# Optimization experiments

Measured on AMD Instinct MI355X. Metric: run time of the kernel, lower is better.

The kernel has to match this reference:

```python
import jax, jax.numpy as jnp
import numpy as np

MIN_NORM = 1e-15
PROJ_EPS = 4e-3  # hgcn PoincareBall eps for float32
C = 1.0          # curvature (constant across both layers)


def _norm(x):
    return jnp.clip(jnp.linalg.norm(x, axis=-1, keepdims=True), MIN_NORM)


def _artanh(x):
    return jnp.arctanh(jnp.clip(x, -1.0 + 1e-7, 1.0 - 1e-7))


def proj(x, c):
    # clip points inside the Poincare ball of curvature c
    n = _norm(x)
    maxnorm = (1.0 - PROJ_EPS) / jnp.sqrt(c)
    return jnp.where(n > maxnorm, x / n * maxnorm, x)


def expmap0(u, c):
    sc = jnp.sqrt(c)
    n = _norm(u)
    return jnp.tanh(sc * n) * u / (sc * n)


def logmap0(p, c):
    sc = jnp.sqrt(c)
    n = _norm(p)
    return _artanh(sc * n) * p / (sc * n)


def mobius_add(x, y, c):
    x2 = jnp.sum(x * x, -1, keepdims=True)
    y2 = jnp.sum(y * y, -1, keepdims=True)
    xy = jnp.sum(x * y, -1, keepdims=True)
    num = (1.0 + 2.0 * c * xy + c * y2) * x + (1.0 - c * x2) * y
    den = 1.0 + 2.0 * c * xy + (c ** 2) * x2 * y2
    return num / jnp.clip(den, MIN_NORM)


def mobius_matvec(W, x, c):
    sc = jnp.sqrt(c)
    xn = _norm(x)
    mx = x @ W.T
    mxn = _norm(mx)
    res = jnp.tanh(mxn / xn * _artanh(sc * xn)) * mx / (mxn * sc)
    zero = jnp.all(mx == 0, axis=-1, keepdims=True)
    return jnp.where(zero, jnp.zeros((), x.dtype), res)


def hgc_layer(x, W, b, src, dst, ew, c_in, c_out, N):
    # HypLinear: mobius matvec + hyperbolic bias
    h = proj(mobius_matvec(W, x, c_in), c_in)
    hyp_b = proj(expmap0(b[None, :], c_in), c_in)  # proj_tan0 is identity
    h = proj(mobius_add(h, hyp_b, c_in), c_in)
    # HypAgg: tangent-space sparse aggregation
    xt = logmap0(h, c_in)                               # [N, d]
    msg = ew[:, None] * xt[src]                          # [E, d] gather
    agg = jax.ops.segment_sum(msg, dst, num_segments=N)  # spmm(adj, xt)
    h = proj(expmap0(agg, c_in), c_in)
    # HypAct: relu in tangent space, remap with c_out
    xt = jax.nn.relu(logmap0(h, c_in))
    return proj(expmap0(xt, c_out), c_out)


def setup_inputs() -> dict:
    key = jax.random.key(0)
    ks = jax.random.split(key, 8)
    N, F, H, D, E = 100000, 128, 128, 128, 1600000
    s = 1.0 / np.sqrt(F)
    x = jax.random.normal(ks[0], (N, F), jnp.float32) * 0.1
    W1 = jax.random.normal(ks[1], (H, F), jnp.float32) * s
    b1 = jax.random.normal(ks[2], (H,), jnp.float32) * 0.01
    W2 = jax.random.normal(ks[3], (D, H), jnp.float32) * s
    b2 = jax.random.normal(ks[4], (D,), jnp.float32) * 0.01
    edge_weight = jax.random.uniform(ks[5], (E,), jnp.float32) * (1.0 / 16.0)
    src = jax.random.randint(ks[6], (E,), 0, N)
    dst = jax.random.randint(ks[7], (E,), 0, N)
    return {"x": x, "W1": W1, "b1": b1, "W2": W2, "b2": b2,
            "edge_weight": edge_weight, "src": src, "dst": dst}


def reference(x, W1, b1, W2, b2, edge_weight, src, dst):
    N = x.shape[0]
    # HGCN.encode: map Euclidean features onto the manifold
    xh = proj(expmap0(x, C), C)  # proj_tan0 is identity for PoincareBall
    h = hgc_layer(xh, W1, b1, src, dst, edge_weight, C, C, N)
    h = hgc_layer(h, W2, b2, src, dst, edge_weight, C, C, N)
    return h
```

## Files before the change

kernel.cpp:

```cpp
#include <hip/hip_runtime.h>
#include <hip/hip_bf16.h>

#define MINN 1e-15f
#define MAXN (1.0f - 4e-3f)
#define ATMAX 3.1063031f

#define NBH 9
#define BNODES 512
#define BCAP 10240
#define BWIN (BCAP + 4 * BNODES)
#define PBE 8192

typedef short short8 __attribute__((ext_vector_type(8)));
typedef float f32x4 __attribute__((ext_vector_type(4)));

__device__ __forceinline__ float wsum(float v) {
    v += __shfl_xor(v, 32, 64);
    v += __shfl_xor(v, 16, 64);
    v += __shfl_xor(v, 8, 64);
    v += __shfl_xor(v, 4, 64);
    v += __shfl_xor(v, 2, 64);
    v += __shfl_xor(v, 1, 64);
    return v;
}

__device__ __forceinline__ void splitf(float f, short& hi, short& lo) {
    unsigned u = __float_as_uint(f);
    hi = (short)(u >> 16);
    float r = f - __uint_as_float(u & 0xffff0000u);
    lo = (short)(__float_as_uint(r) >> 16);
}

__device__ __forceinline__ unsigned packsplit_hi(short ha, short hb) {
    return (unsigned)(unsigned short)ha | ((unsigned)(unsigned short)hb << 16);
}

__device__ __forceinline__ unsigned pack_bf16(float a, float b) {
    unsigned ua = __float_as_uint(a);
    unsigned ub = __float_as_uint(b);
    ua = (ua + 0x7fffu + ((ua >> 16) & 1u)) >> 16;
    ub = (ub + 0x7fffu + ((ub >> 16) & 1u)) & 0xffff0000u;
    return ua | ub;
}

__device__ __forceinline__ float tanh_fast(float x) {
    float e = __expf(2.f * x);
    return (e - 1.f) * __builtin_amdgcn_rcpf(e + 1.f);
}
__device__ __forceinline__ float atanh_fast(float x) {
    return 0.5f * __logf((1.f + x) * __builtin_amdgcn_rcpf(1.f - x));
}

__global__ __launch_bounds__(256) void k_bucket(const int* __restrict__ src, const int* __restrict__ dst,
                                                const float* __restrict__ ew, int* __restrict__ gcur,
                                                int2* __restrict__ staging, int E, int NBUCK) {
    __shared__ int hist[512];
    const int tid = threadIdx.x;
    const int e0 = blockIdx.x * PBE;
    for (int i = tid; i < 512; i += 256) hist[i] = 0;
    __syncthreads();
    #pragma unroll 4
    for (int j = 0; j < PBE / 256; j++) {
        int e = e0 + j * 256 + tid;
        if (e < E) atomicAdd(&hist[dst[e] >> NBH], 1);
    }
    __syncthreads();
    for (int b = tid; b < NBUCK; b += 256) {
        int c = hist[b];
        hist[b] = c ? atomicAdd(&gcur[b], c) : 0;
    }
    __syncthreads();
    #pragma unroll 4
    for (int j = 0; j < PBE / 256; j++) {
        int e = e0 + j * 256 + tid;
        if (e < E) {
            int d = dst[e];
            int bkt = d >> NBH;
            int pos = atomicAdd(&hist[bkt], 1);
            if (pos < BCAP)
                staging[(size_t)bkt * BCAP + pos] =
                    make_int2((src[e] & 0x1FFFF) | ((d & (BNODES - 1)) << 17), __float_as_int(ew[e]));
        }
    }
}

__global__ __launch_bounds__(256) void k_cbuild(const int* __restrict__ gcur, const int2* __restrict__ staging,
                                                int2* __restrict__ csr, int2* __restrict__ rp2, int N) {
    __shared__ int cnt[BNODES];
    __shared__ int base[BNODES];
    __shared__ int sbuf[256];
    const int tid = threadIdx.x;
    const int b = blockIdx.x;
    const int bcnt = min(gcur[b], BCAP);
    const int wbase = b * BWIN;
    const int2* st = staging + (size_t)b * BCAP;

    for (int i = tid; i < BNODES; i += 256) cnt[i] = 0;
    __syncthreads();
    for (int i = tid; i < bcnt; i += 256) {
        int nl = (st[i].x >> 17) & (BNODES - 1);
        atomicAdd(&cnt[nl], 1);
    }
    __syncthreads();
    int p0 = (cnt[2 * tid] + 3) & ~3;
    int p1 = (cnt[2 * tid + 1] + 3) & ~3;
    int s = p0 + p1;
    sbuf[tid] = s;
    __syncthreads();
    for (int off = 1; off < 256; off <<= 1) {
        int add = (tid >= off) ? sbuf[tid - off] : 0;
        __syncthreads();
        sbuf[tid] += add;
        __syncthreads();
    }
    int excl = sbuf[tid] - s;
    base[2 * tid] = excl;
    base[2 * tid + 1] = excl + p0;
    __syncthreads();
    for (int i = tid; i < BNODES; i += 256) {
        int node = b * BNODES + i;
        int c = cnt[i];
        int pd = (c + 3) & ~3;
        int gb = wbase + base[i];
        if (node < N) rp2[node] = make_int2(gb, pd);
        for (int k = c; k < pd; k++) csr[gb + k] = make_int2(0, 0);
    }
    __syncthreads();
    for (int i = tid; i < BNODES; i += 256) cnt[i] = wbase + base[i];
    __syncthreads();
    for (int i = tid; i < bcnt; i += 256) {
        int2 p = st[i];
        int nl = (p.x >> 17) & (BNODES - 1);
        int pos = atomicAdd(&cnt[nl], 1);
        csr[pos] = make_int2(p.x & 0x1FFFF, p.y);
    }
}

__global__ __launch_bounds__(256) void k_wprep(const float* __restrict__ W1, const float* __restrict__ W2,
                                               unsigned* __restrict__ WH1, unsigned* __restrict__ WL1,
                                               unsigned* __restrict__ WH2, unsigned* __restrict__ WL2) {
    int i = (blockIdx.x & 31) * 256 + threadIdx.x;
    const float* W = (blockIdx.x < 32) ? W1 : W2;
    unsigned* WH = (blockIdx.x < 32) ? WH1 : WH2;
    unsigned* WL = (blockIdx.x < 32) ? WL1 : WL2;
    float a = W[2 * i], b = W[2 * i + 1];
    short ha, la, hb, lb;
    splitf(a, ha, la); splitf(b, hb, lb);
    WH[i] = packsplit_hi(ha, hb);
    WL[i] = packsplit_hi(la, lb);
}

__global__ __launch_bounds__(64) void k_bias(const float* __restrict__ B1, const float* __restrict__ B2,
                                             float2* __restrict__ HB) {
    const int lane = threadIdx.x;
    const float* B = (blockIdx.x == 0) ? B1 : B2;
    float2 bb = *(const float2*)(B + 2 * lane);
    float nb2 = wsum(bb.x * bb.x + bb.y * bb.y);
    float nb = fmaxf(sqrtf(nb2), MINN);
    float tbc = fminf(tanh_fast(nb), MAXN);
    float fb = tbc / nb;
    HB[blockIdx.x * 65 + lane] = make_float2(fb * bb.x, fb * bb.y);
    if (lane == 0) HB[blockIdx.x * 65 + 64] = make_float2(tbc * tbc, 0.f);
}

template <int ENCODE>
__global__ __launch_bounds__(256) void k_linear(
    const float* __restrict__ X,
    const unsigned* __restrict__ XH, const unsigned* __restrict__ XL,
    const unsigned* __restrict__ WH, const unsigned* __restrict__ WL,
    const float2* __restrict__ HB, const float2* __restrict__ NRM,
    unsigned* __restrict__ OUT, int N)
{
    __shared__ float mxs[4][16][132];
    __shared__ float xn2s[4][16];

    const int lane = threadIdx.x & 63;
    const int wid = threadIdx.x >> 6;
    const int lr = lane & 15;
    const int lg = lane >> 4;
    const int tbase = blockIdx.x * 4;

    short8 Bh[2][4], Bl[2][4];
    #pragma unroll
    for (int ct = 0; ct < 2; ct++) {
        const int nrow = wid * 32 + ct * 16 + lr;
        #pragma unroll
        for (int kt = 0; kt < 4; kt++) {
            Bh[ct][kt] = *(const short8*)(WH + nrow * 64 + kt * 16 + lg * 4);
            Bl[ct][kt] = *(const short8*)(WL + nrow * 64 + kt * 16 + lg * 4);
        }
    }
    float2 hb = HB[lane];
    float y2 = HB[64].x;

    #pragma unroll
    for (int t = 0; t < 4; t++) {
        const int row0 = (tbase + t) << 4;
        if (row0 >= N) break;
        const int arow = min(row0 + lr, N - 1);

        short8 Ah[4], Al[4];
        if (ENCODE) {
            float xn2 = 0.f;
            const float* xr = X + (size_t)arow * 128 + lg * 8;
            #pragma unroll
            for (int kt = 0; kt < 4; kt++) {
                float4 a0 = *(const float4*)(xr + kt * 32);
                float4 a1 = *(const float4*)(xr + kt * 32 + 4);
                float av[8] = {a0.x, a0.y, a0.z, a0.w, a1.x, a1.y, a1.z, a1.w};
                #pragma unroll
                for (int i = 0; i < 8; i++) {
                    xn2 = fmaf(av[i], av[i], xn2);
                    short h, l; splitf(av[i], h, l);
                    Ah[kt][i] = h; Al[kt][i] = l;
                }
            }
            xn2 += __shfl_xor(xn2, 16, 64);
            xn2 += __shfl_xor(xn2, 32, 64);
            if (wid == 0 && lane < 16) xn2s[t][lane] = xn2;
        } else {
            #pragma unroll
            for (int kt = 0; kt < 4; kt++) {
                Ah[kt] = *(const short8*)(XH + (size_t)arow * 64 + kt * 16 + lg * 4);
                Al[kt] = *(const short8*)(XL + (size_t)arow * 64 + kt * 16 + lg * 4);
            }
        }

        f32x4 acc0 = {0.f, 0.f, 0.f, 0.f}, acc1 = {0.f, 0.f, 0.f, 0.f};
        #pragma unroll
        for (int kt = 0; kt < 4; kt++) {
            acc0 = __builtin_amdgcn_mfma_f32_16x16x32_bf16(Ah[kt], Bh[0][kt], acc0, 0, 0, 0);
            acc1 = __builtin_amdgcn_mfma_f32_16x16x32_bf16(Ah[kt], Bh[1][kt], acc1, 0, 0, 0);
            acc0 = __builtin_amdgcn_mfma_f32_16x16x32_bf16(Al[kt], Bh[0][kt], acc0, 0, 0, 0);
            acc1 = __builtin_amdgcn_mfma_f32_16x16x32_bf16(Al[kt], Bh[1][kt], acc1, 0, 0, 0);
            acc0 = __builtin_amdgcn_mfma_f32_16x16x32_bf16(Ah[kt], Bl[0][kt], acc0, 0, 0, 0);
            acc1 = __builtin_amdgcn_mfma_f32_16x16x32_bf16(Ah[kt], Bl[1][kt], acc1, 0, 0, 0);
        }

        #pragma unroll
        for (int r = 0; r < 4; r++) {
            mxs[t][lg * 4 + r][wid * 32 + lr] = acc0[r];
            mxs[t][lg * 4 + r][wid * 32 + 16 + lr] = acc1[r];
        }
    }
    __syncthreads();

    float mn2[16], dmb[16];
    float2 mvv[16];
    #pragma unroll
    for (int t = 0; t < 4; t++) {
        #pragma unroll
        for (int r = 0; r < 4; r++) {
            const int q = t * 4 + r;
            mvv[q] = *(const float2*)&mxs[t][wid * 4 + r][2 * lane];
            mn2[q] = mvv[q].x * mvv[q].x + mvv[q].y * mvv[q].y;
            dmb[q] = mvv[q].x * hb.x + mvv[q].y * hb.y;
        }
    }
    #pragma unroll
    for (int s = 32; s; s >>= 1) {
        #pragma unroll
        for (int q = 0; q < 16; q++) {
            mn2[q] += __shfl_xor(mn2[q], s, 64);
            dmb[q] += __shfl_xor(dmb[q], s, 64);
        }
    }
    #pragma unroll
    for (int t = 0; t < 4; t++) {
        #pragma unroll
        for (int r = 0; r < 4; r++) {
            const int q = t * 4 + r;
            const int row = ((tbase + t) << 4) + wid * 4 + r;
            if (row < N) {
                float xn, axn;
                if (ENCODE) {
                    float n0 = fmaxf(sqrtf(xn2s[t][wid * 4 + r]), MINN);
                    xn = n0;
                    axn = fminf(n0, ATMAX);
                } else {
                    float2 nr = NRM[row];
                    xn = fmaxf(nr.x, MINN);
                    axn = nr.y;
                }
                float mxn = fmaxf(sqrtf(mn2[q]), MINN);
                float arg = (mxn / xn) * axn;
                float thc = fminf(tanh_fast(arg), MAXN);
                float f1 = thc / mxn;
                float x2 = thc * thc;
                float xy = f1 * dmb[q];
                float ca = 1.f + 2.f * xy + y2;
                float cb = 1.f - x2;
                float inv = 1.f / fmaxf(1.f + 2.f * xy + x2 * y2, MINN);
                float ng2 = inv * inv * (ca * ca * x2 + 2.f * ca * cb * xy + cb * cb * y2);
                float ng = fmaxf(sqrtf(ng2), MINN);
                float lf = atanh_fast(fminf(ng, MAXN)) / ng;
                float sle = lf * inv;
                float o0 = sle * (ca * f1 * mvv[q].x + cb * hb.x);
                float o1 = sle * (ca * f1 * mvv[q].y + cb * hb.y);
                OUT[(size_t)row * 64 + lane] = pack_bf16(o0, o1);
            }
        }
    }
}

__global__ __launch_bounds__(256) void k_aggact(const unsigned* __restrict__ XT, const int2* __restrict__ rp2,
                                                const int2* __restrict__ csr,
                                                float* __restrict__ OUTF,
                                                unsigned* __restrict__ OUTH, unsigned* __restrict__ OUTL,
                                                float2* __restrict__ NRM, int N, int last) {
    const int lane = threadIdx.x & 63;
    const int wid = threadIdx.x >> 6;
    int node = blockIdx.x * 4 + wid;
    if (node >= N) return;
    int2 rr = rp2[node];
    int b = __builtin_amdgcn_readfirstlane(rr.x);
    int cnt = __builtin_amdgcn_readfirstlane(rr.y);
    int e8 = b + (cnt & ~7);

    float ax[8], ay[8];
    #pragma unroll
    for (int j = 0; j < 8; j++) { ax[j] = 0.f; ay[j] = 0.f; }

    for (int i = b; i < e8; i += 8) {
        int2 c[8];
        #pragma unroll
        for (int j = 0; j < 8; j++) c[j] = csr[i + j];
        unsigned v[8];
        #pragma unroll
        for (int j = 0; j < 8; j++) v[j] = XT[(size_t)c[j].x * 64 + lane];
        #pragma unroll
        for (int j = 0; j < 8; j++) {
            float w = __int_as_float(c[j].y);
            ax[j] = fmaf(w, __uint_as_float(v[j] << 16), ax[j]);
            ay[j] = fmaf(w, __uint_as_float(v[j] & 0xffff0000u), ay[j]);
        }
    }
    if (cnt & 4) {
        int i = e8;
        int2 c[4];
        #pragma unroll
        for (int j = 0; j < 4; j++) c[j] = csr[i + j];
        unsigned v[4];
        #pragma unroll
        for (int j = 0; j < 4; j++) v[j] = XT[(size_t)c[j].x * 64 + lane];
        #pragma unroll
        for (int j = 0; j < 4; j++) {
            float w = __int_as_float(c[j].y);
            ax[j] = fmaf(w, __uint_as_float(v[j] << 16), ax[j]);
            ay[j] = fmaf(w, __uint_as_float(v[j] & 0xffff0000u), ay[j]);
        }
    }
    float a0 = ((ax[0] + ax[1]) + (ax[2] + ax[3])) + ((ax[4] + ax[5]) + (ax[6] + ax[7]));
    float a1 = ((ay[0] + ay[1]) + (ay[2] + ay[3])) + ((ay[4] + ay[5]) + (ay[6] + ay[7]));

    float r0 = fmaxf(a0, 0.f), r1 = fmaxf(a1, 0.f);
    float n2 = a0 * a0 + a1 * a1;
    float q2 = r0 * r0 + r1 * r1;
    #pragma unroll
    for (int s = 32; s; s >>= 1) {
        n2 += __shfl_xor(n2, s, 64);
        q2 += __shfl_xor(q2, s, 64);
    }
    float n = fmaxf(sqrtf(n2), MINN);
    float cp = fminf(n, ATMAX) / n;
    float nq = fmaxf(cp * sqrtf(q2), MINN);
    float tq = fminf(tanh_fast(nq), MAXN);
    float f2 = tq / nq;
    float sc = f2 * cp;
    float o0 = sc * r0, o1 = sc * r1;
    if (last) {
        *(float2*)(OUTF + (size_t)node * 128 + 2 * lane) = make_float2(o0, o1);
    } else {
        short h0, l0, h1, l1;
        splitf(o0, h0, l0); splitf(o1, h1, l1);
        OUTH[(size_t)node * 64 + lane] = packsplit_hi(h0, h1);
        OUTL[(size_t)node * 64 + lane] = packsplit_hi(l0, l1);
        if (lane == 0) NRM[node] = make_float2(tq, fminf(nq, ATMAX));
    }
}

extern "C" void kernel_launch(void* const* d_in, const int* in_sizes, int n_in,
                              void* d_out, int out_size, void* d_ws, size_t ws_size,
                              hipStream_t stream) {
    const float* x  = (const float*)d_in[0];
    const float* W1 = (const float*)d_in[1];
    const float* b1 = (const float*)d_in[2];
    const float* W2 = (const float*)d_in[3];
    const float* b2 = (const float*)d_in[4];
    const float* ew = (const float*)d_in[5];
    const int* src  = (const int*)d_in[6];
    const int* dst  = (const int*)d_in[7];
    const int N = in_sizes[0] / 128;
    const int E = in_sizes[5];
    float* out = (float*)d_out;

    const int NBUCK = (N + BNODES - 1) >> NBH;
    const int EB = (E + PBE - 1) / PBE;

    char* w = (char*)d_ws;
    unsigned* xt  = (unsigned*)w; w += (size_t)N * 64 * 4;
    unsigned* xh  = (unsigned*)w; w += (size_t)N * 64 * 4;
    unsigned* xl  = (unsigned*)w; w += (size_t)N * 64 * 4;
    int2*   csr   = (int2*)w;   w += (size_t)NBUCK * BWIN * 8;
    float2* nrm   = (float2*)w; w += (size_t)N * 8;
    int2*   rp2   = (int2*)w;   w += (size_t)N * 8;
    int2*   staging = (int2*)w; w += (size_t)NBUCK * BCAP * 8;
    unsigned* wh1 = (unsigned*)w; w += 8192 * 4;
    unsigned* wl1 = (unsigned*)w; w += 8192 * 4;
    unsigned* wh2 = (unsigned*)w; w += 8192 * 4;
    unsigned* wl2 = (unsigned*)w; w += 8192 * 4;
    float2* hbuf  = (float2*)w; w += 2 * 65 * 8;
    int*    gcur  = (int*)w;    w += (size_t)NBUCK * 4 + 256;

    hipMemsetAsync(gcur, 0, (size_t)NBUCK * 4, stream);
    k_bucket<<<EB, 256, 0, stream>>>(src, dst, ew, gcur, staging, E, NBUCK);
    k_cbuild<<<NBUCK, 256, 0, stream>>>(gcur, staging, csr, rp2, N);
    k_wprep<<<64, 256, 0, stream>>>(W1, W2, wh1, wl1, wh2, wl2);
    k_bias<<<2, 64, 0, stream>>>(b1, b2, hbuf);

    const int rowblocks = (N + 3) / 4;
    const int ntiles = (N + 15) / 16;
    const int nlb = (ntiles + 3) / 4;

    k_linear<1><<<nlb, 256, 0, stream>>>(x, nullptr, nullptr, wh1, wl1, hbuf, nullptr, xt, N);
    k_aggact<<<rowblocks, 256, 0, stream>>>(xt, rp2, csr, nullptr, xh, xl, nrm, N, 0);
    k_linear<0><<<nlb, 256, 0, stream>>>(nullptr, xh, xl, wh2, wl2, hbuf + 65, nrm, xt, N);
    k_aggact<<<rowblocks, 256, 0, stream>>>(xt, rp2, csr, out, nullptr, nullptr, nullptr, N, 1);
}
```

Measured before the change: 310.3 us.

## Keep MFMA results in registers and reduce row norms via partial shuffles

After: 300.9 us. 3.0% less time.

```diff
diff --git a/kernel.cpp b/kernel.cpp
--- a/kernel.cpp
+++ b/kernel.cpp
@@ -171,8 +171,8 @@
     const float2* __restrict__ HB, const float2* __restrict__ NRM,
     unsigned* __restrict__ OUT, int N)
 {
-    __shared__ float mxs[4][16][132];
-    __shared__ float xn2s[4][16];
+    __shared__ float pmn[4][16][4];
+    __shared__ float pdm[4][16][4];
 
     const int lane = threadIdx.x & 63;
     const int wid = threadIdx.x >> 6;
@@ -183,15 +183,18 @@
     short8 Bh[2][4], Bl[2][4];
     #pragma unroll
     for (int ct = 0; ct < 2; ct++) {
-        const int nrow = wid * 32 + ct * 16 + lr;
+        const int nrow = wid * 32 + 2 * lr + ct;
         #pragma unroll
         for (int kt = 0; kt < 4; kt++) {
             Bh[ct][kt] = *(const short8*)(WH + nrow * 64 + kt * 16 + lg * 4);
             Bl[ct][kt] = *(const short8*)(WL + nrow * 64 + kt * 16 + lg * 4);
         }
     }
-    float2 hb = HB[lane];
-    float y2 = HB[64].x;
+    const float2 hbc = HB[wid * 16 + lr];
+    const float y2 = HB[64].x;
+
+    f32x4 acc[4][2];
+    float xnr[4];
 
     #pragma unroll
     for (int t = 0; t < 4; t++) {
@@ -217,7 +220,7 @@
             }
             xn2 += __shfl_xor(xn2, 16, 64);
             xn2 += __shfl_xor(xn2, 32, 64);
-            if (wid == 0 && lane < 16) xn2s[t][lane] = xn2;
+            xnr[t] = xn2;
         } else {
             #pragma unroll
             for (int kt = 0; kt < 4; kt++) {
@@ -226,78 +229,90 @@
             }
         }
 
-        f32x4 acc0 = {0.f, 0.f, 0.f, 0.f}, acc1 = {0.f, 0.f, 0.f, 0.f};
+        f32x4 a0 = {0.f, 0.f, 0.f, 0.f}, a1 = {0.f, 0.f, 0.f, 0.f};
         #pragma unroll
         for (int kt = 0; kt < 4; kt++) {
-            acc0 = __builtin_amdgcn_mfma_f32_16x16x32_bf16(Ah[kt], Bh[0][kt], acc0, 0, 0, 0);
-            acc1 = __builtin_amdgcn_mfma_f32_16x16x32_bf16(Ah[kt], Bh[1][kt], acc1, 0, 0, 0);
-            acc0 = __builtin_amdgcn_mfma_f32_16x16x32_bf16(Al[kt], Bh[0][kt], acc0, 0, 0, 0);
-            acc1 = __builtin_amdgcn_mfma_f32_16x16x32_bf16(Al[kt], Bh[1][kt], acc1, 0, 0, 0);
-            acc0 = __builtin_amdgcn_mfma_f32_16x16x32_bf16(Ah[kt], Bl[0][kt], acc0, 0, 0, 0);
-            acc1 = __builtin_amdgcn_mfma_f32_16x16x32_bf16(Ah[kt], Bl[1][kt], acc1, 0, 0, 0);
-        }
-
+            a0 = __builtin_amdgcn_mfma_f32_16x16x32_bf16(Ah[kt], Bh[0][kt], a0, 0, 0, 0);
+            a1 = __builtin_amdgcn_mfma_f32_16x16x32_bf16(Ah[kt], Bh[1][kt], a1, 0, 0, 0);
+            a0 = __builtin_amdgcn_mfma_f32_16x16x32_bf16(Al[kt], Bh[0][kt], a0, 0, 0, 0);
+            a1 = __builtin_amdgcn_mfma_f32_16x16x32_bf16(Al[kt], Bh[1][kt], a1, 0, 0, 0);
+            a0 = __builtin_amdgcn_mfma_f32_16x16x32_bf16(Ah[kt], Bl[0][kt], a0, 0, 0, 0);
+            a1 = __builtin_amdgcn_mfma_f32_16x16x32_bf16(Ah[kt], Bl[1][kt], a1, 0, 0, 0);
+        }
+        acc[t][0] = a0; acc[t][1] = a1;
+
+        float pm[4], pd[4];
         #pragma unroll
         for (int r = 0; r < 4; r++) {
-            mxs[t][lg * 4 + r][wid * 32 + lr] = acc0[r];
-            mxs[t][lg * 4 + r][wid * 32 + 16 + lr] = acc1[r];
-        }
-    }
-    __syncthreads();
-
-    float mn2[16], dmb[16];
-    float2 mvv[16];
+            pm[r] = a0[r] * a0[r] + a1[r] * a1[r];
+            pd[r] = a0[r] * hbc.x + a1[r] * hbc.y;
+        }
+        #pragma unroll
+        for (int s = 1; s <= 8; s <<= 1) {
+            #pragma unroll
+            for (int r = 0; r < 4; r++) {
+                pm[r] += __shfl_xor(pm[r], s, 64);
+                pd[r] += __shfl_xor(pd[r], s, 64);
+            }
+        }
+        if (lr == 0) {
+            #pragma unroll
+            for (int r = 0; r < 4; r++) {
+                pmn[t][lg * 4 + r][wid] = pm[r];
+                pdm[t][lg * 4 + r][wid] = pd[r];
+            }
+        }
+    }
+    __syncthreads();
+
     #pragma unroll
     for (int t = 0; t < 4; t++) {
+        const int row0 = (tbase + t) << 4;
+        if (row0 >= N) break;
+
+        float4 qm = *(const float4*)pmn[t][lr];
+        float4 qd = *(const float4*)pdm[t][lr];
+        float mn2 = (qm.x + qm.y) + (qm.z + qm.w);
+        float dmb = (qd.x + qd.y) + (qd.z + qd.w);
+        const int crow = row0 + lr;
+        float caf1 = 0.f, cbs = 0.f;
+        if (crow < N) {
+            float xn, axn;
+            if (ENCODE) {
+                float n0 = fmaxf(sqrtf(xnr[t]), MINN);
+                xn = n0;
+                axn = fminf(n0, ATMAX);
+            } else {
+                float2 nr = NRM[crow];
+                xn = fmaxf(nr.x, MINN);
+                axn = nr.y;
+            }
+            float mxn = fmaxf(sqrtf(mn2), MINN);
+            float arg = (mxn / xn) * axn;
+            float thc = fminf(tanh_fast(arg), MAXN);
+            float f1 = thc / mxn;
+            float x2 = thc * thc;
+            float xy = f1 * dmb;
+            float ca = 1.f + 2.f * xy + y2;
+            float cb = 1.f - x2;
+            float inv = 1.f / fmaxf(1.f + 2.f * xy + x2 * y2, MINN);
+            float ng2 = inv * inv * (ca * ca * x2 + 2.f * ca * cb * xy + cb * cb * y2);
+            float ng = fmaxf(sqrtf(ng2), MINN);
+            float lf = atanh_fast(fminf(ng, MAXN)) / ng;
+            float sle = lf * inv;
+            caf1 = sle * ca * f1;
+            cbs = sle * cb;
+        }
         #pragma unroll
         for (int r = 0; r < 4; r++) {
-            const int q = t * 4 + r;
-            mvv[q] = *(const float2*)&mxs[t][wid * 4 + r][2 * lane];
-            mn2[q] = mvv[q].x * mvv[q].x + mvv[q].y * mvv[q].y;
-            dmb[q] = mvv[q].x * hb.x + mvv[q].y * hb.y;
-        }
-    }
-    #pragma unroll
-    for (int s = 32; s; s >>= 1) {
-        #pragma unroll
-        for (int q = 0; q < 16; q++) {
-            mn2[q] += __shfl_xor(mn2[q], s, 64);
-            dmb[q] += __shfl_xor(dmb[q], s, 64);
-        }
-    }
-    #pragma unroll
-    for (int t = 0; t < 4; t++) {
-        #pragma unroll
-        for (int r = 0; r < 4; r++) {
-            const int q = t * 4 + r;
-            const int row = ((tbase + t) << 4) + wid * 4 + r;
+            const int q = lg * 4 + r;
+            float c1 = __shfl(caf1, q, 16);
+            float c2 = __shfl(cbs, q, 16);
+            const int row = row0 + q;
             if (row < N) {
-                float xn, axn;
-                if (ENCODE) {
-                    float n0 = fmaxf(sqrtf(xn2s[t][wid * 4 + r]), MINN);
-                    xn = n0;
-                    axn = fminf(n0, ATMAX);
-                } else {
-                    float2 nr = NRM[row];
-                    xn = fmaxf(nr.x, MINN);
-                    axn = nr.y;
-                }
-                float mxn = fmaxf(sqrtf(mn2[q]), MINN);
-                float arg = (mxn / xn) * axn;
-                float thc = fminf(tanh_fast(arg), MAXN);
-                float f1 = thc / mxn;
-                float x2 = thc * thc;
-                float xy = f1 * dmb[q];
-                float ca = 1.f + 2.f * xy + y2;
-                float cb = 1.f - x2;
-                float inv = 1.f / fmaxf(1.f + 2.f * xy + x2 * y2, MINN);
-                float ng2 = inv * inv * (ca * ca * x2 + 2.f * ca * cb * xy + cb * cb * y2);
-                float ng = fmaxf(sqrtf(ng2), MINN);
-                float lf = atanh_fast(fminf(ng, MAXN)) / ng;
-                float sle = lf * inv;
-                float o0 = sle * (ca * f1 * mvv[q].x + cb * hb.x);
-                float o1 = sle * (ca * f1 * mvv[q].y + cb * hb.y);
-                OUT[(size_t)row * 64 + lane] = pack_bf16(o0, o1);
+                float o0 = c1 * acc[t][0][r] + c2 * hbc.x;
+                float o1 = c1 * acc[t][1][r] + c2 * hbc.y;
+                OUT[(size_t)row * 64 + wid * 16 + lr] = pack_bf16(o0, o1);
             }
         }
     }
```
